# Performance work log

Measured on AMD Instinct MI355X. Metric: run time of the kernel, lower is better.

The kernel has to match this reference:

```python
import jax, jax.numpy as jnp
import numpy as np

D = 256; DFFN = 1024; H = 8; NLVL = 4; NPNT = 4; HD = D // H
BS = 4; NQ = 100; NPTS = 25
SPATIAL = [(128, 128), (64, 64), (32, 32), (16, 16)]
LEN_IN = sum(h * w for h, w in SPATIAL)


def _ln(x, g, b, eps=1e-5):
    m = x.mean(-1, keepdims=True)
    v = ((x - m) ** 2).mean(-1, keepdims=True)
    return (x - m) * jax.lax.rsqrt(v + eps) * g + b


def _mha(q, k, v, w_in, b_in, w_out, b_out):
    # torch nn.MultiheadAttention math, batch-first layout [B,S,D]
    B, Sq, _ = q.shape; Sk = k.shape[1]
    wq, wk, wv = jnp.split(w_in, 3, 0); bq, bk, bv = jnp.split(b_in, 3)
    qh = (q @ wq.T + bq).reshape(B, Sq, H, HD).transpose(0, 2, 1, 3)
    kh = (k @ wk.T + bk).reshape(B, Sk, H, HD).transpose(0, 2, 1, 3)
    vh = (v @ wv.T + bv).reshape(B, Sk, H, HD).transpose(0, 2, 1, 3)
    a = jax.nn.softmax(jnp.einsum('bhqd,bhkd->bhqk', qh, kh) * (1.0 / float(np.sqrt(HD))), -1)
    o = jnp.einsum('bhqk,bhkd->bhqd', a, vh).transpose(0, 2, 1, 3).reshape(B, Sq, D)
    return o @ w_out.T + b_out


def _msdeform(query, ref, src, off_w, off_b, aw_w, aw_b, val_w, val_b, out_w, out_b):
    # MSDeformAttn: per-query multi-level bilinear sampling + weighted aggregation
    bs, Lq, _ = query.shape
    value = (src @ val_w.T + val_b).reshape(bs, LEN_IN, H, HD)
    off = (query @ off_w.T + off_b).reshape(bs, Lq, H, NLVL, NPNT, 2)
    aw = jax.nn.softmax((query @ aw_w.T + aw_b).reshape(bs, Lq, H, NLVL * NPNT), -1)
    aw = aw.reshape(bs, Lq, H, NLVL, NPNT)
    norm = jnp.array([[w, h] for h, w in SPATIAL], jnp.float32)  # (W,H) per level
    loc = ref[:, :, None, :, None, :] + off / norm[None, None, None, :, None, :]
    out = jnp.zeros((bs, H, Lq, HD), query.dtype)
    start = 0
    for l, (hh, ww) in enumerate(SPATIAL):
        v_l = value[:, start:start + hh * ww].transpose(0, 2, 1, 3)  # [bs,H,hw,HD]
        start += hh * ww
        # grid_sample align_corners=False pixel coords: loc*size - 0.5
        x = (loc[:, :, :, l, :, 0] * ww - 0.5).transpose(0, 2, 1, 3).reshape(bs, H, Lq * NPNT)
        y = (loc[:, :, :, l, :, 1] * hh - 0.5).transpose(0, 2, 1, 3).reshape(bs, H, Lq * NPNT)
        x0 = jnp.floor(x); y0 = jnp.floor(y); wx = x - x0; wy = y - y0
        x0i = x0.astype(jnp.int32); y0i = y0.astype(jnp.int32); x1i = x0i + 1; y1i = y0i + 1
        def g(xi, yi):
            valid = ((xi >= 0) & (xi < ww) & (yi >= 0) & (yi < hh)).astype(query.dtype)
            idx = jnp.clip(yi, 0, hh - 1) * ww + jnp.clip(xi, 0, ww - 1)
            return jnp.take_along_axis(v_l, idx[..., None], axis=2) * valid[..., None]
        s = (g(x0i, y0i) * ((1 - wx) * (1 - wy))[..., None]
             + g(x1i, y0i) * (wx * (1 - wy))[..., None]
             + g(x0i, y1i) * ((1 - wx) * wy)[..., None]
             + g(x1i, y1i) * (wx * wy)[..., None])
        s = s.reshape(bs, H, Lq, NPNT, HD)
        out = out + (s * aw[:, :, :, l].transpose(0, 2, 1, 3)[..., None]).sum(3)
    return out.transpose(0, 2, 1, 3).reshape(bs, Lq, D) @ out_w.T + out_b


def _fwd(tgt, query_pos, reference_points, src,
         w_in_intra, b_in_intra, w_out_intra, b_out_intra, g_norm_intra, b_norm_intra,
         w_in_inter, b_in_inter, w_out_inter, b_out_inter, g_norm_inter, b_norm_inter,
         off_w, off_b, aw_w, aw_b, val_w, val_b, co_w, co_b, g_norm_cross, b_norm_cross,
         lin1_w, lin1_b, lin2_w, lin2_b, g_norm3, b_norm3):
    bs, nq, npts, d = tgt.shape
    # intra-instance self-attention (over control points)
    q = (tgt + query_pos).reshape(bs * nq, npts, d)
    t2 = _mha(q, q, tgt.reshape(bs * nq, npts, d), w_in_intra, b_in_intra, w_out_intra, b_out_intra)
    tgt = _ln(tgt + t2.reshape(bs, nq, npts, d), g_norm_intra, b_norm_intra)
    # inter-instance self-attention (over queries), no pos embed per source code
    ti = tgt.transpose(0, 2, 1, 3).reshape(bs * npts, nq, d)
    t2 = _mha(ti, ti, ti, w_in_inter, b_in_inter, w_out_inter, b_out_inter)
    ti = _ln(ti + t2, g_norm_inter, b_norm_inter).reshape(bs, npts, nq, d).transpose(0, 2, 1, 3)
    # deformable cross-attention
    ref = jnp.broadcast_to(reference_points[:, :, None], (bs, nq, npts, NLVL, 2)).reshape(bs, nq * npts, NLVL, 2)
    qc = (ti + query_pos).reshape(bs, nq * npts, d)
    t2 = _msdeform(qc, ref, src, off_w, off_b, aw_w, aw_b, val_w, val_b, co_w, co_b).reshape(bs, nq, npts, d)
    tgt = _ln(ti + t2, g_norm_cross, b_norm_cross)
    # FFN
    ff = jax.nn.relu(tgt @ lin1_w.T + lin1_b) @ lin2_w.T + lin2_b
    return _ln(tgt + ff, g_norm3, b_norm3)


def setup_inputs() -> dict:
    key = jax.random.key(0)
    ki = iter(jax.random.split(key, 40))
    def rn(shape, sc=0.02):
        return jax.random.normal(next(ki), shape, jnp.float32) * sc
    inp = dict(
        tgt=jax.random.normal(next(ki), (BS, NQ, NPTS, D), jnp.float32),
        query_pos=jax.random.normal(next(ki), (BS, NQ, NPTS, D), jnp.float32),
        reference_points=jax.random.uniform(next(ki), (BS, NQ, NLVL, 2), jnp.float32),
        src=jax.random.normal(next(ki), (BS, LEN_IN, D), jnp.float32),
        w_in_intra=rn((3 * D, D)), b_in_intra=jnp.zeros((3 * D,), jnp.float32),
        w_out_intra=rn((D, D)), b_out_intra=jnp.zeros((D,), jnp.float32),
        g_norm_intra=jnp.ones((D,), jnp.float32), b_norm_intra=jnp.zeros((D,), jnp.float32),
        w_in_inter=rn((3 * D, D)), b_in_inter=jnp.zeros((3 * D,), jnp.float32),
        w_out_inter=rn((D, D)), b_out_inter=jnp.zeros((D,), jnp.float32),
        g_norm_inter=jnp.ones((D,), jnp.float32), b_norm_inter=jnp.zeros((D,), jnp.float32),
        off_w=rn((H * NLVL * NPNT * 2, D), 0.001), off_b=rn((H * NLVL * NPNT * 2,), 0.5),
        aw_w=rn((H * NLVL * NPNT, D)), aw_b=jnp.zeros((H * NLVL * NPNT,), jnp.float32),
        val_w=rn((D, D)), val_b=jnp.zeros((D,), jnp.float32),
        co_w=rn((D, D)), co_b=jnp.zeros((D,), jnp.float32),
        g_norm_cross=jnp.ones((D,), jnp.float32), b_norm_cross=jnp.zeros((D,), jnp.float32),
        lin1_w=rn((DFFN, D)), lin1_b=jnp.zeros((DFFN,), jnp.float32),
        lin2_w=rn((D, DFFN)), lin2_b=jnp.zeros((D,), jnp.float32),
        g_norm3=jnp.ones((D,), jnp.float32), b_norm3=jnp.zeros((D,), jnp.float32),
        src_spatial_shapes=jnp.array(SPATIAL, jnp.int32),
        level_start_index=jnp.array(np.cumsum([0] + [h * w for h, w in SPATIAL[:-1]]), jnp.int32),
    )
    return inp


def reference(tgt, query_pos, reference_points, src,
              w_in_intra, b_in_intra, w_out_intra, b_out_intra, g_norm_intra, b_norm_intra,
              w_in_inter, b_in_inter, w_out_inter, b_out_inter, g_norm_inter, b_norm_inter,
              off_w, off_b, aw_w, aw_b, val_w, val_b, co_w, co_b, g_norm_cross, b_norm_cross,
              lin1_w, lin1_b, lin2_w, lin2_b, g_norm3, b_norm3,
              src_spatial_shapes, level_start_index):
    # spatial shapes / level starts are compile-time constants (SPATIAL); args kept for signature parity
    return _fwd(tgt, query_pos, reference_points, src,
                w_in_intra, b_in_intra, w_out_intra, b_out_intra, g_norm_intra, b_norm_intra,
                w_in_inter, b_in_inter, w_out_inter, b_out_inter, g_norm_inter, b_norm_inter,
                off_w, off_b, aw_w, aw_b, val_w, val_b, co_w, co_b, g_norm_cross, b_norm_cross,
                lin1_w, lin1_b, lin2_w, lin2_b, g_norm3, b_norm3)
```

## Files before the change

### kernel.cpp

```cpp
#include <hip/hip_runtime.h>
#include <math.h>

#define DMODEL 256
#define HEADS  8
#define HDIM   32
#define BS     4
#define NQ     100
#define NPTS   25
#define LQ     2500
#define M10K   10000
#define LEN_IN 21760
#define MVAL   87040

typedef float f32x4 __attribute__((ext_vector_type(4)));
typedef short s16x8 __attribute__((ext_vector_type(8)));
typedef unsigned short u16;

static __device__ __forceinline__ short f2bf(float f) {
    unsigned u = __builtin_bit_cast(unsigned, f);
    u = (u + 0x7fffu + ((u >> 16) & 1u)) >> 16;
    return (short)u;
}
static __device__ __forceinline__ unsigned pack2(float lo, float hi) {
    return (unsigned)(u16)f2bf(lo) | ((unsigned)(u16)f2bf(hi) << 16);
}
static __device__ __forceinline__ float bf_lo(unsigned u) {
    return __builtin_bit_cast(float, u << 16);
}
static __device__ __forceinline__ float bf_hi(unsigned u) {
    return __builtin_bit_cast(float, u & 0xffff0000u);
}

#define LDSK   40
#define LDSK64 72

static __device__ __forceinline__ void body_value64_wf32(
    char* smem_, const float* __restrict__ A, const float* __restrict__ Wf,
    const float* __restrict__ bias, u16* __restrict__ C, int bx, int by)
{
    short* As = (short*)smem_;
    short* Ws = (short*)(smem_ + 5120);

    const int tid = threadIdx.x;
    const int n0 = bx * 128;
    const int m0 = by * 64;

    const int arow = tid >> 2;
    const int ak = (tid & 3) * 8;
    const int wrow = tid >> 1;
    const int wk = (tid & 1) * 16;

    const float* aptr = A + (size_t)(m0 + arow) * 256 + ak;
    const float* wptr = Wf + (size_t)(n0 + wrow) * 256 + wk;

    const int wave = tid >> 6;
    const int wm = wave & 1, wn = wave >> 1;
    const int lane = tid & 63;
    const int lrow = lane & 15, kq = lane >> 4;

    f32x4 acc[2][4];
#pragma unroll
    for (int i = 0; i < 2; ++i)
#pragma unroll
        for (int j = 0; j < 4; ++j) acc[i][j] = (f32x4)(0.f);

    float4 pa0 = *(const float4*)aptr;
    float4 pa1 = *(const float4*)(aptr + 4);
    float4 pw0 = *(const float4*)(wptr);
    float4 pw1 = *(const float4*)(wptr + 4);
    float4 pw2 = *(const float4*)(wptr + 8);
    float4 pw3 = *(const float4*)(wptr + 12);

    for (int k0 = 0; k0 < 256; k0 += 32) {
        s16x8 av, wv0, wv1;
        av[0]=f2bf(pa0.x); av[1]=f2bf(pa0.y); av[2]=f2bf(pa0.z); av[3]=f2bf(pa0.w);
        av[4]=f2bf(pa1.x); av[5]=f2bf(pa1.y); av[6]=f2bf(pa1.z); av[7]=f2bf(pa1.w);
        wv0[0]=f2bf(pw0.x); wv0[1]=f2bf(pw0.y); wv0[2]=f2bf(pw0.z); wv0[3]=f2bf(pw0.w);
        wv0[4]=f2bf(pw1.x); wv0[5]=f2bf(pw1.y); wv0[6]=f2bf(pw1.z); wv0[7]=f2bf(pw1.w);
        wv1[0]=f2bf(pw2.x); wv1[1]=f2bf(pw2.y); wv1[2]=f2bf(pw2.z); wv1[3]=f2bf(pw2.w);
        wv1[4]=f2bf(pw3.x); wv1[5]=f2bf(pw3.y); wv1[6]=f2bf(pw3.z); wv1[7]=f2bf(pw3.w);
        *(s16x8*)&As[arow * LDSK + ak]     = av;
        *(s16x8*)&Ws[wrow * LDSK + wk]     = wv0;
        *(s16x8*)&Ws[wrow * LDSK + wk + 8] = wv1;
        __syncthreads();
        if (k0 + 32 < 256) {
            pa0 = *(const float4*)(aptr + k0 + 32);
            pa1 = *(const float4*)(aptr + k0 + 36);
            pw0 = *(const float4*)(wptr + k0 + 32);
            pw1 = *(const float4*)(wptr + k0 + 36);
            pw2 = *(const float4*)(wptr + k0 + 40);
            pw3 = *(const float4*)(wptr + k0 + 44);
        }

        s16x8 af[2], bfv[4];
#pragma unroll
        for (int i = 0; i < 2; ++i)
            af[i] = *(const s16x8*)&As[(wm * 32 + i * 16 + lrow) * LDSK + kq * 8];
#pragma unroll
        for (int j = 0; j < 4; ++j)
            bfv[j] = *(const s16x8*)&Ws[(wn * 64 + j * 16 + lrow) * LDSK + kq * 8];
#pragma unroll
        for (int i = 0; i < 2; ++i)
#pragma unroll
            for (int j = 0; j < 4; ++j)
                acc[i][j] = __builtin_amdgcn_mfma_f32_16x16x32_bf16(af[i], bfv[j], acc[i][j], 0, 0, 0);
        __syncthreads();
    }

#pragma unroll
    for (int i = 0; i < 2; ++i)
#pragma unroll
        for (int j = 0; j < 4; ++j) {
            int col = n0 + wn * 64 + j * 16 + lrow;
            float bv = bias[col];
#pragma unroll
            for (int reg = 0; reg < 4; ++reg) {
                int gmo = m0 + wm * 32 + i * 16 + kq * 4 + reg;
                C[(size_t)gmo * 256 + col] = (u16)f2bf(acc[i][j][reg] + bv);
            }
        }
}

__global__ __launch_bounds__(256) void fat_stage0_kernel(
    const float* __restrict__ s0, const float* __restrict__ s1,
    const float* __restrict__ s2, const float* __restrict__ s3,
    const float* __restrict__ s4, const float* __restrict__ s5,
    const float* __restrict__ s6, const float* __restrict__ s7,
    const float* __restrict__ s8, const float* __restrict__ s9,
    u16* __restrict__ dst,
    const float* __restrict__ a, const float* __restrict__ b,
    u16* __restrict__ xb, u16* __restrict__ ab,
    const float* __restrict__ src, const float* __restrict__ valwf,
    const float* __restrict__ valb, u16* __restrict__ valueb)
{
    __shared__ __align__(16) char smem0[15360];
    if (blockIdx.x < 624) {
        int t8 = (blockIdx.x * 256 + threadIdx.x) * 8;
        if (t8 >= 1277952) return;
        const float* s; int base;
        if      (t8 <  196608) { s = s0; base = 0;       }
        else if (t8 <  262144) { s = s1; base = 196608;  }
        else if (t8 <  458752) { s = s2; base = 262144;  }
        else if (t8 <  524288) { s = s3; base = 458752;  }
        else if (t8 <  589824) { s = s4; base = 524288;  }
        else if (t8 <  622592) { s = s5; base = 589824;  }
        else if (t8 <  688128) { s = s6; base = 622592;  }
        else if (t8 <  753664) { s = s7; base = 688128;  }
        else if (t8 < 1015808) { s = s8; base = 753664;  }
        else                   { s = s9; base = 1015808; }
        const float* p = s + (t8 - base);
        float4 fa = *(const float4*)p;
        float4 fb = *(const float4*)(p + 4);
        s16x8 v;
        v[0]=f2bf(fa.x); v[1]=f2bf(fa.y); v[2]=f2bf(fa.z); v[3]=f2bf(fa.w);
        v[4]=f2bf(fb.x); v[5]=f2bf(fb.y); v[6]=f2bf(fb.z); v[7]=f2bf(fb.w);
        *(s16x8*)(dst + t8) = v;
    } else if (blockIdx.x < 1874) {
        int i = (blockIdx.x - 624) * 256 + threadIdx.x;
        size_t o = (size_t)i * 8;
        float4 a0 = *(const float4*)(a + o);
        float4 a1 = *(const float4*)(a + o + 4);
        s16x8 v;
        v[0]=f2bf(a0.x); v[1]=f2bf(a0.y); v[2]=f2bf(a0.z); v[3]=f2bf(a0.w);
        v[4]=f2bf(a1.x); v[5]=f2bf(a1.y); v[6]=f2bf(a1.z); v[7]=f2bf(a1.w);
        *(s16x8*)(ab + o) = v;
        float4 b0 = *(const float4*)(b + o);
        float4 b1 = *(const float4*)(b + o + 4);
        a0.x += b0.x; a0.y += b0.y; a0.z += b0.z; a0.w += b0.w;
        a1.x += b1.x; a1.y += b1.y; a1.z += b1.z; a1.w += b1.w;
        s16x8 w;
        w[0]=f2bf(a0.x); w[1]=f2bf(a0.y); w[2]=f2bf(a0.z); w[3]=f2bf(a0.w);
        w[4]=f2bf(a1.x); w[5]=f2bf(a1.y); w[6]=f2bf(a1.z); w[7]=f2bf(a1.w);
        *(s16x8*)(xb + o) = w;
    } else {
        const int vb = blockIdx.x - 1874;
        body_value64_wf32(smem0, src, valwf, valb, valueb, vb & 1, vb >> 1);
    }
}


static __device__ __forceinline__ void body_mfma128(
    char* smem_, const u16* __restrict__ A, const u16* __restrict__ W,
    const float* __restrict__ bias, u16* __restrict__ Cv, int bx, int by)
{
    short* As = (short*)smem_;
    short* Ws = (short*)(smem_ + 10240);

    const int tid = threadIdx.x;
    const int m0 = by * 128, n0 = bx * 128;
    const int srow = tid >> 1;
    const int sk = (tid & 1) * 16;
    const int wave = tid >> 6;
    const int wm = wave & 1, wn = wave >> 1;
    const int lane = tid & 63;
    const int lrow = lane & 15, kq = lane >> 4;

    const int gm = m0 + srow;
    const u16* aptr = A + (size_t)gm * 256 + sk;
    const u16* wptr = W + (size_t)(n0 + srow) * 256 + sk;

    f32x4 acc[4][4];
#pragma unroll
    for (int i = 0; i < 4; ++i)
#pragma unroll
        for (int j = 0; j < 4; ++j) acc[i][j] = (f32x4)(0.f);

    s16x8 a0 = (s16x8)0, a1 = (s16x8)0, w0, w1;
    if (gm < M10K) { a0 = *(const s16x8*)aptr; a1 = *(const s16x8*)(aptr + 8); }
    w0 = *(const s16x8*)wptr; w1 = *(const s16x8*)(wptr + 8);

    for (int k0 = 0; k0 < 256; k0 += 32) {
        *(s16x8*)&As[srow * LDSK + sk]     = a0;
        *(s16x8*)&As[srow * LDSK + sk + 8] = a1;
        *(s16x8*)&Ws[srow * LDSK + sk]     = w0;
        *(s16x8*)&Ws[srow * LDSK + sk + 8] = w1;
        __syncthreads();
        if (k0 + 32 < 256) {
            if (gm < M10K) {
                a0 = *(const s16x8*)(aptr + k0 + 32);
                a1 = *(const s16x8*)(aptr + k0 + 40);
            }
            w0 = *(const s16x8*)(wptr + k0 + 32);
            w1 = *(const s16x8*)(wptr + k0 + 40);
        }

        s16x8 af[4], bfv[4];
#pragma unroll
        for (int i = 0; i < 4; ++i)
            af[i] = *(const s16x8*)&As[(wm * 64 + i * 16 + lrow) * LDSK + kq * 8];
#pragma unroll
        for (int j = 0; j < 4; ++j)
            bfv[j] = *(const s16x8*)&Ws[(wn * 64 + j * 16 + lrow) * LDSK + kq * 8];
#pragma unroll
        for (int i = 0; i < 4; ++i)
#pragma unroll
            for (int j = 0; j < 4; ++j)
                acc[i][j] = __builtin_amdgcn_mfma_f32_16x16x32_bf16(af[i], bfv[j], acc[i][j], 0, 0, 0);
        __syncthreads();
    }

#pragma unroll
    for (int i = 0; i < 4; ++i)
#pragma unroll
        for (int j = 0; j < 4; ++j) {
            int col = n0 + wn * 64 + j * 16 + lrow;
            float bv = bias[col];
#pragma unroll
            for (int reg = 0; reg < 4; ++reg) {
                int gmo = m0 + wm * 64 + i * 16 + kq * 4 + reg;
                if (gmo < M10K)
                    Cv[(size_t)gmo * 768 + col] = (u16)f2bf(acc[i][j][reg] + bv);
            }
        }
}

static __device__ __forceinline__ void body_mfma64(
    char* smem_, const u16* __restrict__ A, const u16* __restrict__ W,
    const float* __restrict__ bias, u16* __restrict__ Cv, int bx, int by)
{
    short* As = (short*)smem_;
    short* Ws = (short*)(smem_ + 9216);

    const int tid = threadIdx.x;
    const int m0 = by * 64, n0 = bx * 64;
    const int srow = tid >> 2;
    const int sk = (tid & 3) * 16;
    const int wave = tid >> 6;
    const int wm = wave & 1, wn = wave >> 1;
    const int lane = tid & 63;
    const int lrow = lane & 15, kq = lane >> 4;

    const int gm = m0 + srow;
    const u16* aptr = A + (size_t)gm * 256 + sk;
    const u16* wptr = W + (size_t)(n0 + srow) * 256 + sk;

    f32x4 acc[2][2];
#pragma unroll
    for (int i = 0; i < 2; ++i)
#pragma unroll
        for (int j = 0; j < 2; ++j) acc[i][j] = (f32x4)(0.f);

    s16x8 a0 = (s16x8)0, a1 = (s16x8)0, w0, w1;
    if (gm < M10K) { a0 = *(const s16x8*)aptr; a1 = *(const s16x8*)(aptr + 8); }
    w0 = *(const s16x8*)wptr; w1 = *(const s16x8*)(wptr + 8);

    for (int k0 = 0; k0 < 256; k0 += 64) {
        *(s16x8*)&As[srow * LDSK64 + sk]     = a0;
        *(s16x8*)&As[srow * LDSK64 + sk + 8] = a1;
        *(s16x8*)&Ws[srow * LDSK64 + sk]     = w0;
        *(s16x8*)&Ws[srow * LDSK64 + sk + 8] = w1;
        __syncthreads();
        if (k0 + 64 < 256) {
            if (gm < M10K) {
                a0 = *(const s16x8*)(aptr + k0 + 64);
                a1 = *(const s16x8*)(aptr + k0 + 72);
            }
            w0 = *(const s16x8*)(wptr + k0 + 64);
            w1 = *(const s16x8*)(wptr + k0 + 72);
        }

#pragma unroll
        for (int s = 0; s < 2; ++s) {
            s16x8 af[2], bfv[2];
#pragma unroll
            for (int i = 0; i < 2; ++i)
                af[i] = *(const s16x8*)&As[(wm * 32 + i * 16 + lrow) * LDSK64 + s * 32 + kq * 8];
#pragma unroll
            for (int j = 0; j < 2; ++j)
                bfv[j] = *(const s16x8*)&Ws[(wn * 32 + j * 16 + lrow) * LDSK64 + s * 32 + kq * 8];
#pragma unroll
            for (int i = 0; i < 2; ++i)
#pragma unroll
                for (int j = 0; j < 2; ++j)
                    acc[i][j] = __builtin_amdgcn_mfma_f32_16x16x32_bf16(af[i], bfv[j], acc[i][j], 0, 0, 0);
        }
        __syncthreads();
    }

#pragma unroll
    for (int i = 0; i < 2; ++i)
#pragma unroll
        for (int j = 0; j < 2; ++j) {
            int col = n0 + wn * 32 + j * 16 + lrow;
            float bv = bias[col];
#pragma unroll
            for (int reg = 0; reg < 4; ++reg) {
                int gmo = m0 + wm * 32 + i * 16 + kq * 4 + reg;
                if (gmo < M10K)
                    Cv[(size_t)gmo * 768 + col] = (u16)f2bf(acc[i][j][reg] + bv);
            }
        }
}

__global__ __launch_bounds__(256) void fat_stage1_kernel(
    const u16* __restrict__ x1b, const u16* __restrict__ wqk,
    const float* __restrict__ bqk, u16* __restrict__ qkvb,
    const u16* __restrict__ tgtb, const u16* __restrict__ wv,
    const float* __restrict__ bv, u16* __restrict__ qkvb_v)
{
    __shared__ __align__(16) char smem[20480];
    const int b = blockIdx.x;
    if (b < 316) {
        body_mfma128(smem, x1b, wqk, bqk, qkvb, b & 3, b >> 2);
    } else {
        const int bb = b - 316;
        body_mfma64(smem, tgtb, wv, bv, qkvb_v, bb & 3, bb >> 2);
    }
}

__global__ __launch_bounds__(256) void gemm_mfma_kernel(
    const u16* __restrict__ A, int lda,
    const u16* __restrict__ W, int K,
    const float* __restrict__ bias,
    void* __restrict__ Cv, int ldc,
    int M, int relu, int out_bf16,
    int ncut, const float* __restrict__ bias2,
    float* __restrict__ Cv2, int ldc2)
{
    __shared__ short As[64 * LDSK64];
    __shared__ short Ws[64 * LDSK64];

    const int tid = threadIdx.x;
    const int m0 = blockIdx.y * 64, n0 = blockIdx.x * 64;
    const int srow = tid >> 2;
    const int sk = (tid & 3) * 16;
    const int wave = tid >> 6;
    const int wm = wave & 1, wn = wave >> 1;
    const int lane = tid & 63;
    const int lrow = lane & 15;
    const int kq = lane >> 4;

    const int gm = m0 + srow;
    const u16* aptr = A + (size_t)gm * lda + sk;
    const u16* wptr = W + (size_t)(n0 + srow) * K + sk;

    f32x4 acc[2][2];
#pragma unroll
    for (int i = 0; i < 2; ++i)
#pragma unroll
        for (int j = 0; j < 2; ++j) acc[i][j] = (f32x4)(0.f);

    s16x8 a0 = (s16x8)0, a1 = (s16x8)0, w0, w1;
    if (gm < M) { a0 = *(const s16x8*)aptr; a1 = *(const s16x8*)(aptr + 8); }
    w0 = *(const s16x8*)wptr; w1 = *(const s16x8*)(wptr + 8);

    for (int k0 = 0; k0 < K; k0 += 64) {
        *(s16x8*)&As[srow * LDSK64 + sk]     = a0;
        *(s16x8*)&As[srow * LDSK64 + sk + 8] = a1;
        *(s16x8*)&Ws[srow * LDSK64 + sk]     = w0;
        *(s16x8*)&Ws[srow * LDSK64 + sk + 8] = w1;
        __syncthreads();
        if (k0 + 64 < K) {
            if (gm < M) {
                a0 = *(const s16x8*)(aptr + k0 + 64);
                a1 = *(const s16x8*)(aptr + k0 + 72);
            }
            w0 = *(const s16x8*)(wptr + k0 + 64);
            w1 = *(const s16x8*)(wptr + k0 + 72);
        }

#pragma unroll
        for (int s = 0; s < 2; ++s) {
            s16x8 af[2], bfv[2];
#pragma unroll
            for (int i = 0; i < 2; ++i)
                af[i] = *(const s16x8*)&As[(wm * 32 + i * 16 + lrow) * LDSK64 + s * 32 + kq * 8];
#pragma unroll
            for (int j = 0; j < 2; ++j)
                bfv[j] = *(const s16x8*)&Ws[(wn * 32 + j * 16 + lrow) * LDSK64 + s * 32 + kq * 8];
#pragma unroll
            for (int i = 0; i < 2; ++i)
#pragma unroll
                for (int j = 0; j < 2; ++j)
                    acc[i][j] = __builtin_amdgcn_mfma_f32_16x16x32_bf16(af[i], bfv[j], acc[i][j], 0, 0, 0);
        }
        __syncthreads();
    }

#pragma unroll
    for (int i = 0; i < 2; ++i)
#pragma unroll
        for (int j = 0; j < 2; ++j) {
            int col = n0 + wn * 32 + j * 16 + lrow;
            float bv = (col < ncut) ? bias[col] : bias2[col - ncut];
#pragma unroll
            for (int reg = 0; reg < 4; ++reg) {
                int gmo = m0 + wm * 32 + i * 16 + kq * 4 + reg;
                if (gmo < M) {
                    float v = acc[i][j][reg] + bv;
                    if (relu) v = fmaxf(v, 0.f);
                    if (col < ncut) {
                        if (out_bf16)
                            ((u16*)Cv)[(size_t)gmo * ldc + col] = (u16)f2bf(v);
                        else
                            ((float*)Cv)[(size_t)gmo * ldc + col] = v;
                    } else {
                        Cv2[(size_t)gmo * ldc2 + (col - ncut)] = v;
                    }
                }
            }
        }
}

__global__ __launch_bounds__(256) void gemm_mfma128_kernel(
    const u16* __restrict__ A, int lda,
    const u16* __restrict__ W, int K,
    const float* __restrict__ bias,
    void* __restrict__ Cv, int ldc,
    int M, int relu, int out_bf16)
{
    __shared__ short As[128 * LDSK64];
    __shared__ short Ws[128 * LDSK64];

    const int tid = threadIdx.x;
    const int m0 = blockIdx.y * 128, n0 = blockIdx.x * 128;

    const int srow = tid >> 1;
    const int sk = (tid & 1) * 32;

    const int wave = tid >> 6;
    const int wm = wave & 1, wn = wave >> 1;
    const int lane = tid & 63;
    const int lrow = lane & 15;
    const int kq = lane >> 4;

    const int gm = m0 + srow;
    const u16* aptr = A + (size_t)gm * lda + sk;
    const u16* wptr = W + (size_t)(n0 + srow) * K + sk;

    f32x4 acc[4][4];
#pragma unroll
    for (int i = 0; i < 4; ++i)
#pragma unroll
        for (int j = 0; j < 4; ++j) acc[i][j] = (f32x4)(0.f);

    s16x8 a0 = (s16x8)0, a1 = (s16x8)0, a2 = (s16x8)0, a3 = (s16x8)0;
    s16x8 w0, w1, w2, w3;
    if (gm < M) {
        a0 = *(const s16x8*)aptr;        a1 = *(const s16x8*)(aptr + 8);
        a2 = *(const s16x8*)(aptr + 16); a3 = *(const s16x8*)(aptr + 24);
    }
    w0 = *(const s16x8*)wptr;        w1 = *(const s16x8*)(wptr + 8);
    w2 = *(const s16x8*)(wptr + 16); w3 = *(const s16x8*)(wptr + 24);

    for (int k0 = 0; k0 < K; k0 += 64) {
        *(s16x8*)&As[srow * LDSK64 + sk]      = a0;
        *(s16x8*)&As[srow * LDSK64 + sk + 8]  = a1;
        *(s16x8*)&As[srow * LDSK64 + sk + 16] = a2;
        *(s16x8*)&As[srow * LDSK64 + sk + 24] = a3;
        *(s16x8*)&Ws[srow * LDSK64 + sk]      = w0;
        *(s16x8*)&Ws[srow * LDSK64 + sk + 8]  = w1;
        *(s16x8*)&Ws[srow * LDSK64 + sk + 16] = w2;
        *(s16x8*)&Ws[srow * LDSK64 + sk + 24] = w3;
        __syncthreads();
        if (k0 + 64 < K) {
            if (gm < M) {
                a0 = *(const s16x8*)(aptr + k0 + 64);
                a1 = *(const s16x8*)(aptr + k0 + 72);
                a2 = *(const s16x8*)(aptr + k0 + 80);
                a3 = *(const s16x8*)(aptr + k0 + 88);
            }
            w0 = *(const s16x8*)(wptr + k0 + 64);
            w1 = *(const s16x8*)(wptr + k0 + 72);
            w2 = *(const s16x8*)(wptr + k0 + 80);
            w3 = *(const s16x8*)(wptr + k0 + 88);
        }

#pragma unroll
        for (int s = 0; s < 2; ++s) {
            s16x8 af[4], bfv[4];
#pragma unroll
            for (int i = 0; i < 4; ++i)
                af[i] = *(const s16x8*)&As[(wm * 64 + i * 16 + lrow) * LDSK64 + s * 32 + kq * 8];
#pragma unroll
            for (int j = 0; j < 4; ++j)
                bfv[j] = *(const s16x8*)&Ws[(wn * 64 + j * 16 + lrow) * LDSK64 + s * 32 + kq * 8];
#pragma unroll
            for (int i = 0; i < 4; ++i)
#pragma unroll
                for (int j = 0; j < 4; ++j)
                    acc[i][j] = __builtin_amdgcn_mfma_f32_16x16x32_bf16(af[i], bfv[j], acc[i][j], 0, 0, 0);
        }
        __syncthreads();
    }

#pragma unroll
    for (int i = 0; i < 4; ++i)
#pragma unroll
        for (int j = 0; j < 4; ++j) {
            int col = n0 + wn * 64 + j * 16 + lrow;
            float bv = bias[col];
#pragma unroll
            for (int reg = 0; reg < 4; ++reg) {
                int gmo = m0 + wm * 64 + i * 16 + kq * 4 + reg;
                if (gmo < M) {
                    float v = acc[i][j][reg] + bv;
                    if (relu) v = fmaxf(v, 0.f);
                    if (out_bf16)
                        ((u16*)Cv)[(size_t)gmo * ldc + col] = (u16)f2bf(v);
                    else
                        ((float*)Cv)[(size_t)gmo * ldc + col] = v;
                }
            }
        }
}

__global__ __launch_bounds__(256) void inter_attn_mfma_kernel(
    const u16* __restrict__ qkv, u16* __restrict__ out, float scale)
{
    __shared__ __align__(16) u16 Qs[112 * 40];
    __shared__ __align__(16) u16 Ks[112 * 40];
    __shared__ __align__(16) u16 Vt[32 * 136];
    __shared__ __align__(16) u16 Ps[112 * 136];

    const int b = blockIdx.x, h = blockIdx.y;
    const u16* base = qkv + (size_t)b * 100 * 768;
    const int tid = threadIdx.x;
    const int wave = tid >> 6, lane = tid & 63;
    const int lr = lane & 15, quad = lane >> 4;

    for (int i = tid; i < 12 * 20; i += 256) {
        int row = 100 + i / 20, c = (i % 20) * 2;
        *(unsigned*)&Qs[row * 40 + c] = 0;
        *(unsigned*)&Ks[row * 40 + c] = 0;
    }
    for (int i = tid; i < 2176; i += 256) ((unsigned*)Vt)[i] = 0;
    for (int i = tid; i < 7616; i += 256) ((unsigned*)Ps)[i] = 0;
    __syncthreads();

    for (int idx = tid; idx < 2400; idx += 256) {
        int row = idx / 24, s = idx % 24;
        const u16* p = (s < 8)  ? base + row * 768 + h * 32 + s * 4
                     : (s < 16) ? base + row * 768 + 256 + h * 32 + (s - 8) * 4
                                : base + row * 768 + 512 + h * 32 + (s - 16) * 4;
        if (s < 8) {
            *(uint2*)&Qs[row * 40 + s * 4] = *(const uint2*)p;
        } else if (s < 16) {
            *(uint2*)&Ks[row * 40 + (s - 8) * 4] = *(const uint2*)p;
        } else {
            int d0 = (s - 16) * 4;
            Vt[(d0 + 0) * 136 + row] = p[0];
            Vt[(d0 + 1) * 136 + row] = p[1];
            Vt[(d0 + 2) * 136 + row] = p[2];
            Vt[(d0 + 3) * 136 + row] = p[3];
        }
    }
    __syncthreads();

#pragma unroll 1
    for (int rr = 0; rr < 2; ++rr) {
        int rt = wave + rr * 4;
        if (rt < 7) {
            s16x8 aq = *(const s16x8*)&Qs[(rt * 16 + lr) * 40 + quad * 8];
            f32x4 sc[7];
#pragma unroll
            for (int ct = 0; ct < 7; ++ct) {
                s16x8 bk = *(const s16x8*)&Ks[(ct * 16 + lr) * 40 + quad * 8];
                sc[ct] = __builtin_amdgcn_mfma_f32_16x16x32_bf16(aq, bk, (f32x4)(0.f), 0, 0, 0);
            }
            const bool colok[7] = {true, true, true, true, true, true, (lr < 4)};
#pragma unroll
            for (int reg = 0; reg < 4; ++reg) {
                float mx = -1e30f;
#pragma unroll
                for (int ct = 0; ct < 7; ++ct) {
                    float sv = sc[ct][reg] * scale;
                    sc[ct][reg] = sv;
                    if (colok[ct]) mx = fmaxf(mx, sv);
                }
#pragma unroll
                for (int d = 1; d < 16; d <<= 1) mx = fmaxf(mx, __shfl_xor(mx, d));
                float ssum = 0.f;
#pragma unroll
                for (int ct = 0; ct < 7; ++ct) {
                    float pv = colok[ct] ? __expf(sc[ct][reg] - mx) : 0.f;
                    sc[ct][reg] = pv;
                    ssum += pv;
                }
#pragma unroll
                for (int d = 1; d < 16; d <<= 1) ssum += __shfl_xor(ssum, d);
                float inv = 1.f / ssum;
                int prow = rt * 16 + quad * 4 + reg;
#pragma unroll
                for (int ct = 0; ct < 7; ++ct)
                    Ps[prow * 136 + ct * 16 + lr] = (u16)f2bf(sc[ct][reg] * inv);
            }
        }
    }
    __syncthreads();

#pragma unroll 1
    for (int rr = 0; rr < 2; ++rr) {
        int rt = wave + rr * 4;
        if (rt < 7) {
            f32x4 o0 = (f32x4)(0.f), o1 = (f32x4)(0.f);
#pragma unroll
            for (int kk = 0; kk < 4; ++kk) {
                s16x8 ap = *(const s16x8*)&Ps[(rt * 16 + lr) * 136 + kk * 32 + quad * 8];
                s16x8 bv0 = *(const s16x8*)&Vt[lr * 136 + kk * 32 + quad * 8];
                s16x8 bv1 = *(const s16x8*)&Vt[(16 + lr) * 136 + kk * 32 + quad * 8];
                o0 = __builtin_amdgcn_mfma_f32_16x16x32_bf16(ap, bv0, o0, 0, 0, 0);
                o1 = __builtin_amdgcn_mfma_f32_16x16x32_bf16(ap, bv1, o1, 0, 0, 0);
            }
#pragma unroll
            for (int reg = 0; reg < 4; ++reg) {
                int q = rt * 16 + quad * 4 + reg;
                if (q < 100) {
                    u16* op = out + ((size_t)b * 100 + q) * 256 + h * 32;
                    op[lr]      = (u16)f2bf(o0[reg]);
                    op[16 + lr] = (u16)f2bf(o1[reg]);
                }
            }
        }
    }
}

__global__ __launch_bounds__(256) void intra_fused_kernel(
    const u16* __restrict__ qkv,
    const u16* __restrict__ W,
    const float* __restrict__ bias,
    const float* __restrict__ res,
    const float* __restrict__ g, const float* __restrict__ beta,
    float* __restrict__ outf, u16* __restrict__ outbf,
    float scale)
{
    __shared__ __align__(16) uint2 KVh[25][128];
    __shared__ __align__(16) u16 Ao[32 * 264];
    __shared__ short Ws[256 * LDSK];
    __shared__ float redS[4][32];
    __shared__ float redV[4][32];

    const int inst = blockIdx.x;
    const int tid = threadIdx.x;
    const int h = tid >> 5, r = tid & 31;
    const u16* base = qkv + (size_t)inst * 25 * 768;

    for (int i = tid; i < 7 * 132; i += 256)
        ((unsigned*)&Ao[25 * 264])[i] = 0;
    for (int idx = tid; idx < 3200; idx += 256) {
        int row = idx >> 7, c = idx & 127;
        KVh[row][c] = *(const uint2*)(base + row * 768 + 256 + c * 4);
    }

    float q[32];
    if (r < 25) {
        const u16* qp = base + r * 768 + h * 32;
#pragma unroll
        for (int c4 = 0; c4 < 8; ++c4) {
            uint2 u = *(const uint2*)(qp + c4 * 4);
            q[c4*4+0] = bf_lo(u.x); q[c4*4+1] = bf_hi(u.x);
            q[c4*4+2] = bf_lo(u.y); q[c4*4+3] = bf_hi(u.y);
        }
    }
    __syncthreads();

    if (r < 25) {
        float m = -1e30f, l = 0.f, acc[32];
#pragma unroll
        for (int c = 0; c < 32; ++c) acc[c] = 0.f;
#pragma unroll 2
        for (int j = 0; j < 25; ++j) {
            const uint2* kr = &KVh[j][h * 8];
            float dot = 0.f;
#pragma unroll
            for (int c4 = 0; c4 < 8; ++c4) {
                uint2 u = kr[c4];
                dot = fmaf(q[c4*4+0], bf_lo(u.x), dot);
                dot = fmaf(q[c4*4+1], bf_hi(u.x), dot);
                dot = fmaf(q[c4*4+2], bf_lo(u.y), dot);
                dot = fmaf(q[c4*4+3], bf_hi(u.y), dot);
            }
            dot *= scale;
            float mn = fmaxf(m, dot);
            float alpha = __expf(m - mn);
            float p = __expf(dot - mn);
            l = l * alpha + p;
            const uint2* vr = &KVh[j][64 + h * 8];
#pragma unroll
            for (int c4 = 0; c4 < 8; ++c4) {
                uint2 u = vr[c4];
                acc[c4*4+0] = acc[c4*4+0] * alpha + p * bf_lo(u.x);
                acc[c4*4+1] = acc[c4*4+1] * alpha + p * bf_hi(u.x);
                acc[c4*4+2] = acc[c4*4+2] * alpha + p * bf_lo(u.y);
                acc[c4*4+3] = acc[c4*4+3] * alpha + p * bf_hi(u.y);
            }
            m = mn;
        }
        float inv = 1.f / l;
        unsigned* op = (unsigned*)&Ao[r * 264 + h * 32];
#pragma unroll
        for (int c = 0; c < 16; ++c)
            op[c] = pack2(acc[2*c] * inv, acc[2*c+1] * inv);
    }

    const int wave = tid >> 6, lane = tid & 63;
    const int lrow = lane & 15, kq = lane >> 4;

    f32x4 acc2[2][4];
#pragma unroll
    for (int i = 0; i < 2; ++i)
#pragma unroll
        for (int j = 0; j < 4; ++j) acc2[i][j] = (f32x4)(0.f);

    const u16* wptr = W + (size_t)tid * 256;
    for (int k0 = 0; k0 < 256; k0 += 32) {
        __syncthreads();
        *(s16x8*)&Ws[tid * LDSK +  0] = *(const s16x8*)(wptr + k0);
        *(s16x8*)&Ws[tid * LDSK +  8] = *(const s16x8*)(wptr + k0 + 8);
        *(s16x8*)&Ws[tid * LDSK + 16] = *(const s16x8*)(wptr + k0 + 16);
        *(s16x8*)&Ws[tid * LDSK + 24] = *(const s16x8*)(wptr + k0 + 24);
        __syncthreads();

        s16x8 af[2], bfv[4];
#pragma unroll
        for (int i = 0; i < 2; ++i)
            af[i] = *(const s16x8*)&Ao[(i * 16 + lrow) * 264 + k0 + kq * 8];
#pragma unroll
        for (int j = 0; j < 4; ++j)
            bfv[j] = *(const s16x8*)&Ws[(wave * 64 + j * 16 + lrow) * LDSK + kq * 8];
#pragma unroll
        for (int i = 0; i < 2; ++i)
#pragma unroll
            for (int j = 0; j < 4; ++j)
                acc2[i][j] = __builtin_amdgcn_mfma_f32_16x16x32_bf16(af[i], bfv[j], acc2[i][j], 0, 0, 0);
    }

    const int qq = inst % 100, bb = inst / 100;
    float x[2][4][4];
#pragma unroll
    for (int i = 0; i < 2; ++i)
#pragma unroll
        for (int j = 0; j < 4; ++j) {
            const int col = wave * 64 + j * 16 + lrow;
            const float bv = bias[col];
#pragma unroll
            for (int reg = 0; reg < 4; ++reg) {
                const int rowp = i * 16 + kq * 4 + reg;
                float rv = (rowp < 25) ? res[((size_t)inst * 25 + rowp) * 256 + col] : 0.f;
                x[i][j][reg] = rv + (acc2[i][j][reg] + bv);
            }
        }

#pragma unroll
    for (int i = 0; i < 2; ++i)
#pragma unroll
        for (int reg = 0; reg < 4; ++reg) {
            float s = x[i][0][reg] + x[i][1][reg] + x[i][2][reg] + x[i][3][reg];
            s += __shfl_xor(s, 1); s += __shfl_xor(s, 2);
            s += __shfl_xor(s, 4); s += __shfl_xor(s, 8);
            if (lrow == 0) redS[wave][i * 16 + kq * 4 + reg] = s;
        }
    __syncthreads();
    float mean[2][4];
#pragma unroll
    for (int i = 0; i < 2; ++i)
#pragma unroll
        for (int reg = 0; reg < 4; ++reg) {
            const int rowp = i * 16 + kq * 4 + reg;
            mean[i][reg] = (redS[0][rowp] + redS[1][rowp] + redS[2][rowp] + redS[3][rowp]) * (1.f / 256.f);
        }
#pragma unroll
    for (int i = 0; i < 2; ++i)
#pragma unroll
        for (int reg = 0; reg < 4; ++reg) {
            float vs = 0.f;
#pragma unroll
            for (int j = 0; j < 4; ++j) {
                float d = x[i][j][reg] - mean[i][reg];
                vs += d * d;
            }
            vs += __shfl_xor(vs, 1); vs += __shfl_xor(vs, 2);
            vs += __shfl_xor(vs, 4); vs += __shfl_xor(vs, 8);
            if (lrow == 0) redV[wave][i * 16 + kq * 4 + reg] = vs;
        }
    __syncthreads();

#pragma unroll
    for (int i = 0; i < 2; ++i)
#pragma unroll
        for (int reg = 0; reg < 4; ++reg) {
            const int rowp = i * 16 + kq * 4 + reg;
            if (rowp >= 25) continue;
            const float rstd = rsqrtf(
                (redV[0][rowp] + redV[1][rowp] + redV[2][rowp] + redV[3][rowp]) * (1.f / 256.f) + 1e-5f);
            const size_t ro = ((size_t)bb * 25 + rowp) * 100 + qq;
#pragma unroll
            for (int j = 0; j < 4; ++j) {
                const int col = wave * 64 + j * 16 + lrow;
                const float y = (x[i][j][reg] - mean[i][reg]) * rstd * g[col] + beta[col];
                outf[ro * 256 + col] = y;
                outbf[ro * 256 + col] = (u16)f2bf(y);
            }
        }
}

__global__ __launch_bounds__(256) void add_ln_kernel(
    const float* __restrict__ a, const float* __restrict__ b,
    const float* __restrict__ g, const float* __restrict__ beta,
    float* __restrict__ out, u16* __restrict__ out_bf,
    const float* __restrict__ qp, u16* __restrict__ qout,
    int transpose_mode)
{
    const int r = blockIdx.x * 4 + (threadIdx.x >> 6);
    const int lane = threadIdx.x & 63;
    const size_t co = (size_t)r * 256 + lane * 4;

    const float4 av = *(const float4*)(a + co);
    const float4 bv = *(const float4*)(b + co);
    float4 x;
    x.x = av.x + bv.x; x.y = av.y + bv.y; x.z = av.z + bv.z; x.w = av.w + bv.w;

    float s = x.x + x.y + x.z + x.w;
#pragma unroll
    for (int off = 32; off >= 1; off >>= 1) s += __shfl_xor(s, off);
    float mean = s * (1.f / 256.f);

    float dx = x.x - mean, dy = x.y - mean, dz = x.z - mean, dw = x.w - mean;
    float vs = dx * dx + dy * dy + dz * dz + dw * dw;
#pragma unroll
    for (int off = 32; off >= 1; off >>= 1) vs += __shfl_xor(vs, off);
    float rstd = rsqrtf(vs * (1.f / 256.f) + 1e-5f);

    size_t ro = r;
    if (transpose_mode == 1) {
        int q = r % 100; int bp = r / 100; int p = bp % 25; int bb = bp / 25;
        ro = ((size_t)bb * 100 + q) * 25 + p;
    } else if (transpose_mode == 2) {
        int p = r % 25; int t = r / 25; int q = t % 100; int bb = t / 100;
        ro = ((size_t)bb * 25 + p) * 100 + q;
    }
    const size_t oo = ro * 256 + lane * 4;

    const float4 gv = *(const float4*)(g + lane * 4);
    const float4 bt = *(const float4*)(beta + lane * 4);
    float4 y;
    y.x = dx * rstd * gv.x + bt.x;
    y.y = dy * rstd * gv.y + bt.y;
    y.z = dz * rstd * gv.z + bt.z;
    y.w = dw * rstd * gv.w + bt.w;

    *(float4*)(out + oo) = y;
    if (out_bf) {
        uint2 pk = make_uint2(pack2(y.x, y.y), pack2(y.z, y.w));
        *(uint2*)(out_bf + oo) = pk;
    }
    if (qout) {
        const float4 qv = *(const float4*)(qp + oo);
        uint2 pk = make_uint2(pack2(y.x + qv.x, y.y + qv.y),
                              pack2(y.z + qv.z, y.w + qv.w));
        *(uint2*)(qout + oo) = pk;
    }
}

__global__ __launch_bounds__(256, 4) void msdeform_sample_kernel(
    const u16* __restrict__ value,
    const float* __restrict__ off,
    const float* __restrict__ awl,
    const float* __restrict__ refp,
    u16* __restrict__ sampled)
{
    const int unit = blockIdx.x * 8 + (threadIdx.x >> 5);
    const int t = threadIdx.x & 31;
    const int h = t >> 2, c8 = t & 3;
    const int b = unit / LQ, lq = unit - b * LQ;
    const int q = lq / NPTS;

    const float* awp = awl + (size_t)unit * 128 + h * 16;
    float w[16];
    float mx = -1e30f;
#pragma unroll
    for (int k = 0; k < 16; ++k) { w[k] = awp[k]; mx = fmaxf(mx, w[k]); }
    float sum = 0.f;
#pragma unroll
    for (int k = 0; k < 16; ++k) { w[k] = __expf(w[k] - mx); sum += w[k]; }
    const float inv = 1.f / sum;

    const float* offp = off + (size_t)unit * 256 + h * 32;
    const float* rp = refp + ((size_t)b * 100 + q) * 8;
    const u16* vbase = value + (size_t)b * LEN_IN * 256 + h * 32 + c8 * 8;

    float acc[8];
#pragma unroll
    for (int k = 0; k < 8; ++k) acc[k] = 0.f;

    int start = 0;
    const int sz[4] = {128, 64, 32, 16};
#pragma unroll
    for (int l = 0; l < 4; ++l) {
        const int hh = sz[l], ww = sz[l];
        const float rx = rp[l * 2 + 0], ry = rp[l * 2 + 1];
#pragma unroll 2
        for (int pt = 0; pt < 4; ++pt) {
            float ox = offp[(l * 4 + pt) * 2 + 0];
            float oy = offp[(l * 4 + pt) * 2 + 1];
            float x = rx * ww + ox - 0.5f;
            float y = ry * hh + oy - 0.5f;
            float x0f = floorf(x), y0f = floorf(y);
            float wx = x - x0f, wy = y - y0f;
            int x0 = (int)x0f, y0 = (int)y0f;
            int x1 = x0 + 1, y1 = y0 + 1;
            float aw = w[l * 4 + pt] * inv;

            int x0c = min(max(x0, 0), ww - 1), x1c = min(max(x1, 0), ww - 1);
            int y0c = min(max(y0, 0), hh - 1), y1c = min(max(y1, 0), hh - 1);
            float w00 = aw * (1.f - wx) * (1.f - wy);
            float w10 = aw * wx * (1.f - wy);
            float w01 = aw * (1.f - wx) * wy;
            float w11 = aw * wx * wy;
            if (!(x0 >= 0 && x0 < ww)) { w00 = 0.f; w01 = 0.f; }
            if (!(x1 >= 0 && x1 < ww)) { w10 = 0.f; w11 = 0.f; }
            if (!(y0 >= 0 && y0 < hh)) { w00 = 0.f; w10 = 0.f; }
            if (!(y1 >= 0 && y1 < hh)) { w01 = 0.f; w11 = 0.f; }

            uint4 u00 = *(const uint4*)(vbase + (size_t)(start + y0c * ww + x0c) * 256);
            uint4 u10 = *(const uint4*)(vbase + (size_t)(start + y0c * ww + x1c) * 256);
            uint4 u01 = *(const uint4*)(vbase + (size_t)(start + y1c * ww + x0c) * 256);
            uint4 u11 = *(const uint4*)(vbase + (size_t)(start + y1c * ww + x1c) * 256);

#define ACC4(u, wgt) \
            acc[0] = fmaf(wgt, bf_lo(u.x), acc[0]); \
            acc[1] = fmaf(wgt, bf_hi(u.x), acc[1]); \
            acc[2] = fmaf(wgt, bf_lo(u.y), acc[2]); \
            acc[3] = fmaf(wgt, bf_hi(u.y), acc[3]); \
            acc[4] = fmaf(wgt, bf_lo(u.z), acc[4]); \
            acc[5] = fmaf(wgt, bf_hi(u.z), acc[5]); \
            acc[6] = fmaf(wgt, bf_lo(u.w), acc[6]); \
            acc[7] = fmaf(wgt, bf_hi(u.w), acc[7]);
            ACC4(u00, w00); ACC4(u10, w10); ACC4(u01, w01); ACC4(u11, w11);
#undef ACC4
        }
        start += hh * ww;
    }

    uint4 pk;
    pk.x = pack2(acc[0], acc[1]); pk.y = pack2(acc[2], acc[3]);
    pk.z = pack2(acc[4], acc[5]); pk.w = pack2(acc[6], acc[7]);
    *(uint4*)(sampled + (size_t)unit * 256 + h * 32 + c8 * 8) = pk;
}

extern "C" void kernel_launch(void* const* d_in, const int* in_sizes, int n_in,
                              void* d_out, int out_size, void* d_ws, size_t ws_size,
                              hipStream_t stream)
{
    (void)in_sizes; (void)n_in; (void)out_size; (void)ws_size;

    const float* tgt        = (const float*)d_in[0];
    const float* query_pos  = (const float*)d_in[1];
    const float* refp       = (const float*)d_in[2];
    const float* src        = (const float*)d_in[3];
    const float* w_in_intra = (const float*)d_in[4];
    const float* b_in_intra = (const float*)d_in[5];
    const float* w_out_intra= (const float*)d_in[6];
    const float* b_out_intra= (const float*)d_in[7];
    const float* g_ln_intra = (const float*)d_in[8];
    const float* b_ln_intra = (const float*)d_in[9];
    const float* w_in_inter = (const float*)d_in[10];
    const float* b_in_inter = (const float*)d_in[11];
    const float* w_out_inter= (const float*)d_in[12];
    const float* b_out_inter= (const float*)d_in[13];
    const float* g_ln_inter = (const float*)d_in[14];
    const float* b_ln_inter = (const float*)d_in[15];
    const float* off_w      = (const float*)d_in[16];
    const float* off_b      = (const float*)d_in[17];
    const float* aw_w       = (const float*)d_in[18];
    const float* aw_b       = (const float*)d_in[19];
    const float* val_w      = (const float*)d_in[20];
    const float* val_b      = (const float*)d_in[21];
    const float* co_w       = (const float*)d_in[22];
    const float* co_b       = (const float*)d_in[23];
    const float* g_ln_cross = (const float*)d_in[24];
    const float* b_ln_cross = (const float*)d_in[25];
    const float* lin1_w     = (const float*)d_in[26];
    const float* lin1_b     = (const float*)d_in[27];
    const float* lin2_w     = (const float*)d_in[28];
    const float* lin2_b     = (const float*)d_in[29];
    const float* g_ln3      = (const float*)d_in[30];
    const float* b_ln3      = (const float*)d_in[31];

    float* ws    = (float*)d_ws;
    float* qkv   = ws;
    float* tmp   = ws + 7680000;
    u16*   attnb = (u16*)(ws + 10240000);
    float* tgt1  = ws + 11520000;
    float* ti    = ws + 14080000;
    u16*   tib   = (u16*)(ws + 16640000);
    float* tA    = ws + 17920000;
    u16*   qcb   = (u16*)(ws + 20480000);
    u16*   x1b   = (u16*)(ws + 21760000);
    u16*   tgtb  = (u16*)(ws + 23040000);
    float* awl   = ws + 24320000;
    u16*   valueb= (u16*)(ws + 25600000);
    u16*   wb    = (u16*)(ws + 36741120);
    float* out   = (float*)d_out;

    u16* qkvb = (u16*)qkv;

    u16* wb_in_intra  = wb;
    u16* wb_out_intra = wb + 196608;
    u16* wb_in_inter  = wb + 262144;
    u16* wb_out_inter = wb + 458752;
    u16* wb_off       = wb + 524288;
    u16* wb_co        = wb + 688128;
    u16* wb_lin1      = wb + 753664;
    u16* wb_lin2      = wb + 1015808;

    const float scale = 0.17677669529663687f;
    const int MB64  = (M10K + 63) / 64;
    const int MB128 = (M10K + 127) / 128;
    const int NC_OFF = 1 << 30;

    fat_stage0_kernel<<<4594, 256, 0, stream>>>(
        w_in_intra, w_out_intra, w_in_inter, w_out_inter, off_w,
        aw_w, val_w, co_w, lin1_w, lin2_w, wb,
        tgt, query_pos, x1b, tgtb,
        src, val_w, val_b, valueb);

    fat_stage1_kernel<<<944, 256, 0, stream>>>(
        x1b, wb_in_intra, b_in_intra, qkvb,
        tgtb, wb_in_intra + 512 * 256, b_in_intra + 512, qkvb + 512);

    intra_fused_kernel<<<400, 256, 0, stream>>>(qkvb, wb_out_intra, b_out_intra,
                                                tgt, g_ln_intra, b_ln_intra,
                                                ti, tib, scale);

    gemm_mfma128_kernel<<<dim3(6, MB128), 256, 0, stream>>>(tib, 256, wb_in_inter, 256,
                                                            b_in_inter, qkvb, 768, M10K, 0, 1);
    inter_attn_mfma_kernel<<<dim3(100, 8), 256, 0, stream>>>(qkvb, attnb, scale);
    gemm_mfma_kernel<<<dim3(4, MB64), 256, 0, stream>>>(attnb, 256, wb_out_inter, 256,
                                                        b_out_inter, tmp, 256, M10K, 0, 0,
                                                        NC_OFF, b_out_inter, (float*)0, 0);
    add_ln_kernel<<<2500, 256, 0, stream>>>(ti, tmp, g_ln_inter, b_ln_inter,
                                            tA, (u16*)0, query_pos, qcb, 1);

    gemm_mfma_kernel<<<dim3(6, MB64), 256, 0, stream>>>(qcb, 256, wb_off, 256,
                                                        off_b, tgt1, 256, M10K, 0, 0,
                                                        256, aw_b, awl, 128);
    msdeform_sample_kernel<<<1250, 256, 0, stream>>>(valueb, tgt1, awl, refp, attnb);
    gemm_mfma_kernel<<<dim3(4, MB64), 256, 0, stream>>>(attnb, 256, wb_co, 256,
                                                        co_b, tmp, 256, M10K, 0, 0,
                                                        NC_OFF, co_b, (float*)0, 0);
    add_ln_kernel<<<2500, 256, 0, stream>>>(tA, tmp, g_ln_cross, b_ln_cross,
                                            ti, tib, (const float*)0, (u16*)0, 0);

    gemm_mfma128_kernel<<<dim3(8, MB128), 256, 0, stream>>>(tib, 256, wb_lin1, 256,
                                                            lin1_b, valueb, 1024, M10K, 1, 1);
    gemm_mfma_kernel<<<dim3(4, MB64), 256, 0, stream>>>(valueb, 1024, wb_lin2, 1024,
                                                        lin2_b, tmp, 256, M10K, 0, 0,
                                                        NC_OFF, lin2_b, (float*)0, 0);
    add_ln_kernel<<<2500, 256, 0, stream>>>(ti, tmp, g_ln3, b_ln3,
                                            out, (u16*)0, (const float*)0, (u16*)0, 0);
}
```

Measured before the change: 454.5 us.

## Fuse N=256 output GEMMs with residual add and LayerNorm epilogue

Adds a GEMM kernel where each block computes a full 64x256 output row tile, so the residual add, bias and LayerNorm (with the optional transpose, bf16 and query-pos outputs) can run in the epilogue. It replaces three GEMM + add_ln kernel pairs, removing the fp32 tmp round trip and three launches. In exchange each GEMM has only 157 blocks instead of 628, which lowers occupancy and parallelism on a large GPU. The epilogue stores are also scalar and strided rather than float4.

Result: slower. 497.3 us (+9.4%).

```diff
diff --git a/kernel.cpp b/kernel.cpp
--- a/kernel.cpp
+++ b/kernel.cpp
@@ -348,6 +348,121 @@
     }
 }
 
+__global__ __launch_bounds__(256) void gemm_ln64_kernel(
+    const u16* __restrict__ A, int lda,
+    const u16* __restrict__ W, int K,
+    const float* __restrict__ bias,
+    const float* __restrict__ res,
+    const float* __restrict__ g, const float* __restrict__ beta,
+    float* __restrict__ outf, u16* __restrict__ outbf,
+    const float* __restrict__ qp, u16* __restrict__ qout,
+    int tmode)
+{
+    __shared__ short As[64 * LDSK];
+    __shared__ short Ws[256 * LDSK];
+
+    const int tid = threadIdx.x;
+    const int m0 = blockIdx.x * 64;
+    const int wave = tid >> 6, lane = tid & 63;
+    const int lrow = lane & 15, kq = lane >> 4;
+
+    const int arow = tid >> 2, ak = (tid & 3) * 8;
+    const int gm = m0 + arow;
+    const u16* aptr = A + (size_t)gm * lda + ak;
+    const u16* wptr = W + (size_t)tid * K;
+
+    f32x4 acc[16];
+#pragma unroll
+    for (int j = 0; j < 16; ++j) acc[j] = (f32x4)(0.f);
+
+    s16x8 a0 = (s16x8)0, w0, w1, w2, w3;
+    if (gm < M10K) a0 = *(const s16x8*)aptr;
+    w0 = *(const s16x8*)(wptr);
+    w1 = *(const s16x8*)(wptr + 8);
+    w2 = *(const s16x8*)(wptr + 16);
+    w3 = *(const s16x8*)(wptr + 24);
+
+    for (int k0 = 0; k0 < K; k0 += 32) {
+        *(s16x8*)&As[arow * LDSK + ak] = a0;
+        *(s16x8*)&Ws[tid * LDSK +  0] = w0;
+        *(s16x8*)&Ws[tid * LDSK +  8] = w1;
+        *(s16x8*)&Ws[tid * LDSK + 16] = w2;
+        *(s16x8*)&Ws[tid * LDSK + 24] = w3;
+        __syncthreads();
+        if (k0 + 32 < K) {
+            if (gm < M10K) a0 = *(const s16x8*)(aptr + k0 + 32);
+            w0 = *(const s16x8*)(wptr + k0 + 32);
+            w1 = *(const s16x8*)(wptr + k0 + 40);
+            w2 = *(const s16x8*)(wptr + k0 + 48);
+            w3 = *(const s16x8*)(wptr + k0 + 56);
+        }
+
+        s16x8 af = *(const s16x8*)&As[(wave * 16 + lrow) * LDSK + kq * 8];
+#pragma unroll
+        for (int j = 0; j < 16; ++j) {
+            s16x8 bfv = *(const s16x8*)&Ws[(j * 16 + lrow) * LDSK + kq * 8];
+            acc[j] = __builtin_amdgcn_mfma_f32_16x16x32_bf16(af, bfv, acc[j], 0, 0, 0);
+        }
+        __syncthreads();
+    }
+
+    const int rbase = m0 + wave * 16 + kq * 4;
+    float x[4][16];
+#pragma unroll
+    for (int reg = 0; reg < 4; ++reg) {
+        const int r = rbase + reg;
+        const bool ok = (r < M10K);
+#pragma unroll
+        for (int j = 0; j < 16; ++j) {
+            const int col = j * 16 + lrow;
+            const float rv = ok ? res[(size_t)r * 256 + col] : 0.f;
+            x[reg][j] = rv + acc[j][reg] + bias[col];
+        }
+    }
+
+    float mean[4], rstd[4];
+#pragma unroll
+    for (int reg = 0; reg < 4; ++reg) {
+        float s = 0.f;
+#pragma unroll
+        for (int j = 0; j < 16; ++j) s += x[reg][j];
+        s += __shfl_xor(s, 1); s += __shfl_xor(s, 2);
+        s += __shfl_xor(s, 4); s += __shfl_xor(s, 8);
+        mean[reg] = s * (1.f / 256.f);
+        float vs = 0.f;
+#pragma unroll
+        for (int j = 0; j < 16; ++j) {
+            const float d = x[reg][j] - mean[reg];
+            vs += d * d;
+        }
+        vs += __shfl_xor(vs, 1); vs += __shfl_xor(vs, 2);
+        vs += __shfl_xor(vs, 4); vs += __shfl_xor(vs, 8);
+        rstd[reg] = rsqrtf(vs * (1.f / 256.f) + 1e-5f);
+    }
+
+#pragma unroll
+    for (int reg = 0; reg < 4; ++reg) {
+        const int r = rbase + reg;
+        if (r >= M10K) continue;
+        size_t ro = r;
+        if (tmode == 1) {
+            int q = r % 100; int bp = r / 100; int p = bp % 25; int bb = bp / 25;
+            ro = ((size_t)bb * 100 + q) * 25 + p;
+        } else if (tmode == 2) {
+            int p = r % 25; int t = r / 25; int q = t % 100; int bb = t / 100;
+            ro = ((size_t)bb * 25 + p) * 100 + q;
+        }
+#pragma unroll
+        for (int j = 0; j < 16; ++j) {
+            const int col = j * 16 + lrow;
+            const float y = (x[reg][j] - mean[reg]) * rstd[reg] * g[col] + beta[col];
+            outf[ro * 256 + col] = y;
+            if (outbf) outbf[ro * 256 + col] = (u16)f2bf(y);
+            if (qout)  qout[ro * 256 + col] = (u16)f2bf(y + qp[ro * 256 + col]);
+        }
+    }
+}
+
 __global__ __launch_bounds__(256) void gemm_mfma_kernel(
     const u16* __restrict__ A, int lda,
     const u16* __restrict__ W, int K,
@@ -832,64 +947,6 @@
                 outbf[ro * 256 + col] = (u16)f2bf(y);
             }
         }
-}
-
-__global__ __launch_bounds__(256) void add_ln_kernel(
-    const float* __restrict__ a, const float* __restrict__ b,
-    const float* __restrict__ g, const float* __restrict__ beta,
-    float* __restrict__ out, u16* __restrict__ out_bf,
-    const float* __restrict__ qp, u16* __restrict__ qout,
-    int transpose_mode)
-{
-    const int r = blockIdx.x * 4 + (threadIdx.x >> 6);
-    const int lane = threadIdx.x & 63;
-    const size_t co = (size_t)r * 256 + lane * 4;
-
-    const float4 av = *(const float4*)(a + co);
-    const float4 bv = *(const float4*)(b + co);
-    float4 x;
-    x.x = av.x + bv.x; x.y = av.y + bv.y; x.z = av.z + bv.z; x.w = av.w + bv.w;
-
-    float s = x.x + x.y + x.z + x.w;
-#pragma unroll
-    for (int off = 32; off >= 1; off >>= 1) s += __shfl_xor(s, off);
-    float mean = s * (1.f / 256.f);
-
-    float dx = x.x - mean, dy = x.y - mean, dz = x.z - mean, dw = x.w - mean;
-    float vs = dx * dx + dy * dy + dz * dz + dw * dw;
-#pragma unroll
-    for (int off = 32; off >= 1; off >>= 1) vs += __shfl_xor(vs, off);
-    float rstd = rsqrtf(vs * (1.f / 256.f) + 1e-5f);
-
-    size_t ro = r;
-    if (transpose_mode == 1) {
-        int q = r % 100; int bp = r / 100; int p = bp % 25; int bb = bp / 25;
-        ro = ((size_t)bb * 100 + q) * 25 + p;
-    } else if (transpose_mode == 2) {
-        int p = r % 25; int t = r / 25; int q = t % 100; int bb = t / 100;
-        ro = ((size_t)bb * 25 + p) * 100 + q;
-    }
-    const size_t oo = ro * 256 + lane * 4;
-
-    const float4 gv = *(const float4*)(g + lane * 4);
-    const float4 bt = *(const float4*)(beta + lane * 4);
-    float4 y;
-    y.x = dx * rstd * gv.x + bt.x;
-    y.y = dy * rstd * gv.y + bt.y;
-    y.z = dz * rstd * gv.z + bt.z;
-    y.w = dw * rstd * gv.w + bt.w;
-
-    *(float4*)(out + oo) = y;
-    if (out_bf) {
-        uint2 pk = make_uint2(pack2(y.x, y.y), pack2(y.z, y.w));
-        *(uint2*)(out_bf + oo) = pk;
-    }
-    if (qout) {
-        const float4 qv = *(const float4*)(qp + oo);
-        uint2 pk = make_uint2(pack2(y.x + qv.x, y.y + qv.y),
-                              pack2(y.z + qv.z, y.w + qv.w));
-        *(uint2*)(qout + oo) = pk;
-    }
 }
 
 __global__ __launch_bounds__(256, 4) void msdeform_sample_kernel(
@@ -1032,6 +1089,7 @@
     u16*   valueb= (u16*)(ws + 25600000);
     u16*   wb    = (u16*)(ws + 36741120);
     float* out   = (float*)d_out;
+    (void)tmp;
 
     u16* qkvb = (u16*)qkv;
 
@@ -1047,7 +1105,6 @@
     const float scale = 0.17677669529663687f;
     const int MB64  = (M10K + 63) / 64;
     const int MB128 = (M10K + 127) / 128;
-    const int NC_OFF = 1 << 30;
 
     fat_stage0_kernel<<<4594, 256, 0, stream>>>(
         w_in_intra, w_out_intra, w_in_inter, w_out_inter, off_w,
@@ -1066,27 +1123,21 @@
     gemm_mfma128_kernel<<<dim3(6, MB128), 256, 0, stream>>>(tib, 256, wb_in_inter, 256,
                                                             b_in_inter, qkvb, 768, M10K, 0, 1);
     inter_attn_mfma_kernel<<<dim3(100, 8), 256, 0, stream>>>(qkvb, attnb, scale);
-    gemm_mfma_kernel<<<dim3(4, MB64), 256, 0, stream>>>(attnb, 256, wb_out_inter, 256,
-                                                        b_out_inter, tmp, 256, M10K, 0, 0,
-                                                        NC_OFF, b_out_inter, (float*)0, 0);
-    add_ln_kernel<<<2500, 256, 0, stream>>>(ti, tmp, g_ln_inter, b_ln_inter,
-                                            tA, (u16*)0, query_pos, qcb, 1);
+    gemm_ln64_kernel<<<MB64, 256, 0, stream>>>(attnb, 256, wb_out_inter, 256,
+                                               b_out_inter, ti, g_ln_inter, b_ln_inter,
+                                               tA, (u16*)0, query_pos, qcb, 1);
 
     gemm_mfma_kernel<<<dim3(6, MB64), 256, 0, stream>>>(qcb, 256, wb_off, 256,
                                                         off_b, tgt1, 256, M10K, 0, 0,
                                                         256, aw_b, awl, 128);
     msdeform_sample_kernel<<<1250, 256, 0, stream>>>(valueb, tgt1, awl, refp, attnb);
-    gemm_mfma_kernel<<<dim3(4, MB64), 256, 0, stream>>>(attnb, 256, wb_co, 256,
-                                                        co_b, tmp, 256, M10K, 0, 0,
-                                                        NC_OFF, co_b, (float*)0, 0);
-    add_ln_kernel<<<2500, 256, 0, stream>>>(tA, tmp, g_ln_cross, b_ln_cross,
-                                            ti, tib, (const float*)0, (u16*)0, 0);
+    gemm_ln64_kernel<<<MB64, 256, 0, stream>>>(attnb, 256, wb_co, 256,
+                                               co_b, tA, g_ln_cross, b_ln_cross,
+                                               ti, tib, (const float*)0, (u16*)0, 0);
 
     gemm_mfma128_kernel<<<dim3(8, MB128), 256, 0, stream>>>(tib, 256, wb_lin1, 256,
                                                             lin1_b, valueb, 1024, M10K, 1, 1);
-    gemm_mfma_kernel<<<dim3(4, MB64), 256, 0, stream>>>(valueb, 1024, wb_lin2, 1024,
-                                                        lin2_b, tmp, 256, M10K, 0, 0,
-                                                        NC_OFF, lin2_b, (float*)0, 0);
-    add_ln_kernel<<<2500, 256, 0, stream>>>(ti, tmp, g_ln3, b_ln3,
-                                            out, (u16*)0, (const float*)0, (u16*)0, 0);
-}
+    gemm_ln64_kernel<<<MB64, 256, 0, stream>>>(valueb, 1024, wb_lin2, 1024,
+                                               lin2_b, ti, g_ln3, b_ln3,
+                                               out, (u16*)0, (const float*)0, (u16*)0, 0);
+}
```
